# Optimization experiments

Hardware: AMD Instinct MI355X
Metric: run time of the kernel (lower is better)

## Reference

```python
import jax, jax.numpy as jnp
import numpy as np

IN_CH, OUT_CH = 32, 32
MX, MY = 16, 16


def setup_inputs() -> dict:
    key = jax.random.key(0)
    kx, k1r, k1i, k2r, k2i = jax.random.split(key, 5)
    scale = 1.0 / (IN_CH * OUT_CH)
    x = jax.random.normal(kx, (16, IN_CH, 256, 256), dtype=jnp.float32)
    w_shape = (IN_CH, OUT_CH, MX, MY)
    # complex weights stored as real/imag float32 pairs (torch.randn(cfloat) draws
    # independent normal real and imaginary parts)
    w1_real = jax.random.normal(k1r, w_shape, dtype=jnp.float32) * scale
    w1_imag = jax.random.normal(k1i, w_shape, dtype=jnp.float32) * scale
    w2_real = jax.random.normal(k2r, w_shape, dtype=jnp.float32) * scale
    w2_imag = jax.random.normal(k2i, w_shape, dtype=jnp.float32) * scale
    return {"x": x, "w1_real": w1_real, "w1_imag": w1_imag,
            "w2_real": w2_real, "w2_imag": w2_imag}


def reference(x, w1_real, w1_imag, w2_real, w2_imag):
    b, c_in, gx, gy = x.shape
    w1 = w1_real + 1j * w1_imag  # [Cin, Cout, MX, MY]
    w2 = w2_real + 1j * w2_imag
    x_ft = jnp.fft.rfft2(x, axes=(-2, -1))  # [B, Cin, gx, gy//2+1] complex
    # fused complex channel mixing over retained modes (replaces Cin*Cout loop)
    top = jnp.einsum('bixy,ioxy->boxy', x_ft[:, :, :MX, :MY], w1)
    bot = jnp.einsum('bixy,ioxy->boxy', x_ft[:, :, -MX:, :MY], w2)
    out_ft = jnp.zeros((b, OUT_CH, gx, gy // 2 + 1), dtype=x_ft.dtype)
    out_ft = out_ft.at[:, :, :MX, :MY].set(top)
    out_ft = out_ft.at[:, :, -MX:, :MY].set(bot)
    return jnp.fft.irfft2(out_ft, s=(gx, gy), axes=(-2, -1)).astype(x.dtype)
```

## Files before the change

### kernel.cpp

```cpp
#include <hip/hip_runtime.h>
#include <math.h>

#define B     16
#define CIN   32
#define COUT  32
#define G     256
#define NSITE 512

__device__ __forceinline__ int swz8(int bid, int nwg) {
    int q = nwg >> 3;
    return (bid & 7) * q + (bid >> 3);
}

__global__ __launch_bounds__(256, 2) void k_fwd(const float* __restrict__ x,
                                                float2* __restrict__ X) {
    __shared__ float2 tw[256];
    __shared__ float tile[32][257];
    __shared__ float2 T[256][17];
    const int t = threadIdx.x;
    {
        double ang = (double)t * (M_PI / 128.0);
        tw[t] = make_float2((float)cos(ang), (float)sin(ang));
    }
    const int img = blockIdx.x;
    const float* xp = x + (size_t)img * (G * G);

    float ar[16], ai[16], wr[16], wi[16], sr[16], si[16];
    #pragma unroll
    for (int k = 0; k < 16; ++k) { ar[k] = 0.f; ai[k] = 0.f; }
    __syncthreads();
    #pragma unroll
    for (int k = 0; k < 16; ++k) { sr[k] = tw[k].x; si[k] = -tw[k].y; }

    const int row0 = t >> 3, seg = t & 7;
    float4 rs[8];
    #pragma unroll
    for (int p = 0; p < 8; ++p)
        rs[p] = *reinterpret_cast<const float4*>(xp + (size_t)(p * 32 + row0) * G + seg * 4);
    #pragma unroll
    for (int p = 0; p < 8; ++p) {
        int cc = seg * 4, rr = p * 32 + row0;
        tile[cc + 0][rr] = rs[p].x; tile[cc + 1][rr] = rs[p].y;
        tile[cc + 2][rr] = rs[p].z; tile[cc + 3][rr] = rs[p].w;
    }
    __syncthreads();

    for (int c = 0; c < 8; ++c) {
        const int ny0 = c * 32;
        if (c < 7) {
            #pragma unroll
            for (int p = 0; p < 8; ++p)
                rs[p] = *reinterpret_cast<const float4*>(
                    xp + (size_t)(p * 32 + row0) * G + (ny0 + 32) + seg * 4);
        }
        #pragma unroll
        for (int k = 0; k < 16; ++k) {
            float2 w0 = tw[(k * ny0) & 255];
            wr[k] = w0.x; wi[k] = -w0.y;
        }
        for (int j = 0; j < 32; ++j) {
            float xv = tile[j][t];
            #pragma unroll
            for (int k = 0; k < 16; ++k) {
                ar[k] = fmaf(xv, wr[k], ar[k]);
                ai[k] = fmaf(xv, wi[k], ai[k]);
                float nr = fmaf(wr[k], sr[k], -wi[k] * si[k]);
                wi[k]    = fmaf(wr[k], si[k],  wi[k] * sr[k]);
                wr[k] = nr;
            }
        }
        __syncthreads();
        if (c < 7) {
            #pragma unroll
            for (int p = 0; p < 8; ++p) {
                int cc = seg * 4, rr = p * 32 + row0;
                tile[cc + 0][rr] = rs[p].x; tile[cc + 1][rr] = rs[p].y;
                tile[cc + 2][rr] = rs[p].z; tile[cc + 3][rr] = rs[p].w;
            }
            __syncthreads();
        }
    }
    #pragma unroll
    for (int k = 0; k < 16; ++k) T[t][k] = make_float2(ar[k], ai[k]);
    __syncthreads();

    const int ky = t & 15, kxg = t >> 4;
    float x1r = 0.f, x1i = 0.f, x2r = 0.f, x2i = 0.f;
    float w1r = 1.f, w1i = 0.f, w2r = 1.f, w2i = 0.f;
    const float s1r = tw[kxg].x,      s1i = -tw[kxg].y;
    const float s2r = tw[16 - kxg].x, s2i =  tw[16 - kxg].y;
    for (int c = 0; c < 8; ++c) {
        const int nx0 = c * 32;
        {
            int e1 = (kxg * nx0) & 255;
            w1r = tw[e1].x; w1i = -tw[e1].y;
            int e2 = ((16 - kxg) * nx0) & 255;
            w2r = tw[e2].x; w2i = tw[e2].y;
        }
        for (int j = 0; j < 32; ++j) {
            float2 tv = T[nx0 + j][ky];
            x1r = fmaf(tv.x, w1r, fmaf(-tv.y, w1i, x1r));
            x1i = fmaf(tv.x, w1i, fmaf( tv.y, w1r, x1i));
            x2r = fmaf(tv.x, w2r, fmaf(-tv.y, w2i, x2r));
            x2i = fmaf(tv.x, w2i, fmaf( tv.y, w2r, x2i));
            float n1 = fmaf(w1r, s1r, -w1i * s1i);
            w1i      = fmaf(w1r, s1i,  w1i * s1r);
            w1r = n1;
            float n2 = fmaf(w2r, s2r, -w2i * s2i);
            w2i      = fmaf(w2r, s2i,  w2i * s2r);
            w2r = n2;
        }
    }
    float2* Xp = X + (size_t)img * NSITE;
    Xp[kxg * 16 + ky]        = make_float2(x1r, x1i);
    Xp[(kxg + 16) * 16 + ky] = make_float2(x2r, x2i);
}

__global__ __launch_bounds__(256) void k_mix(const float2* __restrict__ X,
                                             const float* __restrict__ w1r,
                                             const float* __restrict__ w1i,
                                             const float* __restrict__ w2r,
                                             const float* __restrict__ w2i,
                                             float2* __restrict__ Y) {
    __shared__ float2 Ws[CIN][COUT];
    __shared__ float2 Xs[B][CIN];
    const int t = threadIdx.x;
    const int site = swz8(blockIdx.x, NSITE);
    const int kxi = site >> 4, kky = site & 15;
    const float* wr; const float* wi; int kxl;
    if (kxi < 16) { wr = w1r; wi = w1i; kxl = kxi; }
    else          { wr = w2r; wi = w2i; kxl = kxi - 16; }
    const int wofs = kxl * 16 + kky;
    for (int p = t; p < CIN * COUT; p += 256)
        Ws[p >> 5][p & 31] = make_float2(wr[p * 256 + wofs], wi[p * 256 + wofs]);
    for (int p = t; p < B * CIN; p += 256) {
        int bb = p >> 5, i = p & 31;
        Xs[bb][i] = X[(size_t)(bb * CIN + i) * NSITE + site];
    }
    __syncthreads();
    for (int p = t; p < B * COUT; p += 256) {
        int bb = p >> 5, o = p & 31;
        float yr = 0.f, yi = 0.f;
        #pragma unroll
        for (int i = 0; i < CIN; ++i) {
            float2 xv = Xs[bb][i];
            float2 wv = Ws[i][o];
            yr = fmaf(xv.x, wv.x, fmaf(-xv.y, wv.y, yr));
            yi = fmaf(xv.x, wv.y, fmaf( xv.y, wv.x, yi));
        }
        Y[(size_t)(bb * COUT + o) * NSITE + site] = make_float2(yr, yi);
    }
}

__global__ __launch_bounds__(256, 2) void k_inv(const float2* __restrict__ Y,
                                                float* __restrict__ out) {
    __shared__ float2 tw[256];
    __shared__ float2 Ys[32][16];
    __shared__ float2 U[256][18];
    const int t = threadIdx.x;
    {
        double ang = (double)t * (M_PI / 128.0);
        tw[t] = make_float2((float)cos(ang), (float)sin(ang));
    }
    const int img = blockIdx.x;
    const float2* yp = Y + (size_t)img * NSITE;
    reinterpret_cast<float4*>(Ys)[t] = reinterpret_cast<const float4*>(yp)[t];
    __syncthreads();

    float ur[16], ui[16];
    #pragma unroll
    for (int k = 0; k < 16; ++k) { ur[k] = 0.f; ui[k] = 0.f; }
    const float str = tw[t].x, sti = tw[t].y;
    float wr = 1.f, wi = 0.f;
    #pragma unroll 2
    for (int kxi = 0; kxi < 16; ++kxi) {
        const float4* yrow = reinterpret_cast<const float4*>(Ys[kxi]);
        #pragma unroll
        for (int q = 0; q < 8; ++q) {
            float4 v = yrow[q];
            ur[2*q]   = fmaf(v.x, wr, fmaf(-v.y, wi, ur[2*q]));
            ui[2*q]   = fmaf(v.x, wi, fmaf( v.y, wr, ui[2*q]));
            ur[2*q+1] = fmaf(v.z, wr, fmaf(-v.w, wi, ur[2*q+1]));
            ui[2*q+1] = fmaf(v.z, wi, fmaf( v.w, wr, ui[2*q+1]));
        }
        float nr = fmaf(wr, str, -wi * sti);
        wi       = fmaf(wr, sti,  wi * str);
        wr = nr;
    }
    {
        int e = (16 * t) & 255;
        wr = tw[e].x; wi = -tw[e].y;
    }
    #pragma unroll 2
    for (int kxi = 16; kxi < 32; ++kxi) {
        const float4* yrow = reinterpret_cast<const float4*>(Ys[kxi]);
        #pragma unroll
        for (int q = 0; q < 8; ++q) {
            float4 v = yrow[q];
            ur[2*q]   = fmaf(v.x, wr, fmaf(-v.y, wi, ur[2*q]));
            ui[2*q]   = fmaf(v.x, wi, fmaf( v.y, wr, ui[2*q]));
            ur[2*q+1] = fmaf(v.z, wr, fmaf(-v.w, wi, ur[2*q+1]));
            ui[2*q+1] = fmaf(v.z, wi, fmaf( v.w, wr, ui[2*q+1]));
        }
        float nr = fmaf(wr, str, -wi * sti);
        wi       = fmaf(wr, sti,  wi * str);
        wr = nr;
    }
    #pragma unroll
    for (int k = 0; k < 16; ++k) U[t][k] = make_float2(ur[k], ui[k]);
    __syncthreads();

    const int wv = t >> 6, ln = t & 63;
    float tc[16], ts[16];
    #pragma unroll
    for (int k = 1; k < 16; ++k) {
        float2 w = tw[(k * ln) & 255];
        tc[k] = 2.f * w.x; ts[k] = 2.f * w.y;
    }
    float* op = out + (size_t)img * (G * G);
    for (int r = 0; r < 64; ++r) {
        const int nx = wv * 64 + r;
        float4 u[8];
        #pragma unroll
        for (int q = 0; q < 8; ++q)
            u[q] = reinterpret_cast<const float4*>(U[nx])[q];
        #pragma unroll
        for (int nb = 0; nb < 4; ++nb) {
            float acc = u[0].x;
            #pragma unroll
            for (int k = 1; k < 16; ++k) {
                float urk = (k & 1) ? u[k >> 1].z : u[k >> 1].x;
                float uik = (k & 1) ? u[k >> 1].w : u[k >> 1].y;
                const int m = (k * nb) & 3;
                if (m == 0)      acc = fmaf(urk, tc[k], fmaf(-uik, ts[k], acc));
                else if (m == 1) acc = fmaf(-urk, ts[k], fmaf(-uik, tc[k], acc));
                else if (m == 2) acc = fmaf(-urk, tc[k], fmaf( uik, ts[k], acc));
                else             acc = fmaf( urk, ts[k], fmaf( uik, tc[k], acc));
            }
            op[(size_t)nx * G + nb * 64 + ln] = acc * (1.0f / 65536.0f);
        }
    }
}

extern "C" void kernel_launch(void* const* d_in, const int* in_sizes, int n_in,
                              void* d_out, int out_size, void* d_ws, size_t ws_size,
                              hipStream_t stream) {
    const float* x   = (const float*)d_in[0];
    const float* w1r = (const float*)d_in[1];
    const float* w1i = (const float*)d_in[2];
    const float* w2r = (const float*)d_in[3];
    const float* w2i = (const float*)d_in[4];
    float* out = (float*)d_out;

    float2* X = (float2*)d_ws;
    float2* Y = X + (size_t)B * CIN * NSITE;

    k_fwd<<<dim3(B * CIN),  dim3(256), 0, stream>>>(x, X);
    k_mix<<<dim3(NSITE),    dim3(256), 0, stream>>>(X, w1r, w1i, w2r, w2i, Y);
    k_inv<<<dim3(B * COUT), dim3(256), 0, stream>>>(Y, out);
}
```

Before: 324.6 us.

## Fold DFT symmetries in forward pass and split inverse kernel across four blocks

The forward row DFT now pairs columns n and n+128 into even/odd sums, so each thread does half the twiddle multiply-accumulates per column. The column DFT pairs rows nx and nx+128 with a sign, which halves the loop. The inverse kernel is split into four blocks per image, each handling 64 output rows, with less register state and a higher occupancy hint. This is meant to cut VALU work and raise parallelism. The cost is more index arithmetic, and the small Y load plus twiddle setup is now repeated four times per image.

```diff
diff --git a/kernel.cpp b/kernel.cpp
--- a/kernel.cpp
+++ b/kernel.cpp
@@ -25,47 +25,55 @@
     const int img = blockIdx.x;
     const float* xp = x + (size_t)img * (G * G);
 
-    float ar[16], ai[16], wr[16], wi[16], sr[16], si[16];
-    #pragma unroll
-    for (int k = 0; k < 16; ++k) { ar[k] = 0.f; ai[k] = 0.f; }
-    __syncthreads();
-    #pragma unroll
-    for (int k = 0; k < 16; ++k) { sr[k] = tw[k].x; si[k] = -tw[k].y; }
-
-    const int row0 = t >> 3, seg = t & 7;
+    float tr[16], ti[16], wr[16], wi[16], sr[16], si[16];
+    #pragma unroll
+    for (int k = 0; k < 16; ++k) { tr[k] = 0.f; ti[k] = 0.f; }
+    __syncthreads();
+    #pragma unroll
+    for (int k = 1; k < 16; ++k) { sr[k] = tw[k].x; si[k] = -tw[k].y; }
+
     float4 rs[8];
     #pragma unroll
-    for (int p = 0; p < 8; ++p)
-        rs[p] = *reinterpret_cast<const float4*>(xp + (size_t)(p * 32 + row0) * G + seg * 4);
-    #pragma unroll
     for (int p = 0; p < 8; ++p) {
-        int cc = seg * 4, rr = p * 32 + row0;
-        tile[cc + 0][rr] = rs[p].x; tile[cc + 1][rr] = rs[p].y;
-        tile[cc + 2][rr] = rs[p].z; tile[cc + 3][rr] = rs[p].w;
+        int idx = p * 256 + t, nx = idx >> 3, sub = idx & 7, h = sub >> 2, q = sub & 3;
+        rs[p] = *reinterpret_cast<const float4*>(xp + (size_t)nx * G + (128 * h + 4 * q));
+    }
+    #pragma unroll
+    for (int p = 0; p < 8; ++p) {
+        int idx = p * 256 + t, nx = idx >> 3, sub = idx & 7, h = sub >> 2, q = sub & 3;
+        int r = 16 * h + 4 * q;
+        tile[r + 0][nx] = rs[p].x; tile[r + 1][nx] = rs[p].y;
+        tile[r + 2][nx] = rs[p].z; tile[r + 3][nx] = rs[p].w;
     }
     __syncthreads();
 
     for (int c = 0; c < 8; ++c) {
-        const int ny0 = c * 32;
+        const int m0 = c * 16;
         if (c < 7) {
             #pragma unroll
-            for (int p = 0; p < 8; ++p)
+            for (int p = 0; p < 8; ++p) {
+                int idx = p * 256 + t, nx = idx >> 3, sub = idx & 7, h = sub >> 2, q = sub & 3;
                 rs[p] = *reinterpret_cast<const float4*>(
-                    xp + (size_t)(p * 32 + row0) * G + (ny0 + 32) + seg * 4);
-        }
-        #pragma unroll
-        for (int k = 0; k < 16; ++k) {
-            float2 w0 = tw[(k * ny0) & 255];
+                    xp + (size_t)nx * G + (m0 + 16 + 128 * h + 4 * q));
+            }
+        }
+        #pragma unroll
+        for (int k = 1; k < 16; ++k) {
+            float2 w0 = tw[(k * m0) & 255];
             wr[k] = w0.x; wi[k] = -w0.y;
         }
-        for (int j = 0; j < 32; ++j) {
-            float xv = tile[j][t];
-            #pragma unroll
-            for (int k = 0; k < 16; ++k) {
-                ar[k] = fmaf(xv, wr[k], ar[k]);
-                ai[k] = fmaf(xv, wi[k], ai[k]);
+        #pragma unroll
+        for (int e = 0; e < 16; ++e) {
+            float x0 = tile[e][t], x1 = tile[16 + e][t];
+            float ev = x0 + x1, od = x0 - x1;
+            tr[0] += ev;
+            #pragma unroll
+            for (int k = 1; k < 16; ++k) {
+                float s_ = (k & 1) ? od : ev;
+                tr[k] = fmaf(s_, wr[k], tr[k]);
+                ti[k] = fmaf(s_, wi[k], ti[k]);
                 float nr = fmaf(wr[k], sr[k], -wi[k] * si[k]);
-                wi[k]    = fmaf(wr[k], si[k],  wi[k] * sr[k]);
+                wi[k]   = fmaf(wr[k], si[k],  wi[k] * sr[k]);
                 wr[k] = nr;
             }
         }
@@ -73,42 +81,45 @@
         if (c < 7) {
             #pragma unroll
             for (int p = 0; p < 8; ++p) {
-                int cc = seg * 4, rr = p * 32 + row0;
-                tile[cc + 0][rr] = rs[p].x; tile[cc + 1][rr] = rs[p].y;
-                tile[cc + 2][rr] = rs[p].z; tile[cc + 3][rr] = rs[p].w;
+                int idx = p * 256 + t, nx = idx >> 3, sub = idx & 7, h = sub >> 2, q = sub & 3;
+                int r = 16 * h + 4 * q;
+                tile[r + 0][nx] = rs[p].x; tile[r + 1][nx] = rs[p].y;
+                tile[r + 2][nx] = rs[p].z; tile[r + 3][nx] = rs[p].w;
             }
             __syncthreads();
         }
     }
     #pragma unroll
-    for (int k = 0; k < 16; ++k) T[t][k] = make_float2(ar[k], ai[k]);
+    for (int k = 0; k < 16; ++k) T[t][k] = make_float2(tr[k], ti[k]);
     __syncthreads();
 
     const int ky = t & 15, kxg = t >> 4;
     float x1r = 0.f, x1i = 0.f, x2r = 0.f, x2i = 0.f;
-    float w1r = 1.f, w1i = 0.f, w2r = 1.f, w2i = 0.f;
+    const float sgn = 1.f - 2.f * (float)(kxg & 1);
     const float s1r = tw[kxg].x,      s1i = -tw[kxg].y;
     const float s2r = tw[16 - kxg].x, s2i =  tw[16 - kxg].y;
-    for (int c = 0; c < 8; ++c) {
-        const int nx0 = c * 32;
-        {
-            int e1 = (kxg * nx0) & 255;
-            w1r = tw[e1].x; w1i = -tw[e1].y;
-            int e2 = ((16 - kxg) * nx0) & 255;
-            w2r = tw[e2].x; w2i = tw[e2].y;
-        }
+    for (int c2 = 0; c2 < 4; ++c2) {
+        const int nx0 = c2 * 32;
+        int e1 = (kxg * nx0) & 255;
+        float w1r_ = tw[e1].x, w1i_ = -tw[e1].y;
+        int e2 = ((16 - kxg) * nx0) & 255;
+        float w2r_ = tw[e2].x, w2i_ = tw[e2].y;
+        #pragma unroll
         for (int j = 0; j < 32; ++j) {
-            float2 tv = T[nx0 + j][ky];
-            x1r = fmaf(tv.x, w1r, fmaf(-tv.y, w1i, x1r));
-            x1i = fmaf(tv.x, w1i, fmaf( tv.y, w1r, x1i));
-            x2r = fmaf(tv.x, w2r, fmaf(-tv.y, w2i, x2r));
-            x2i = fmaf(tv.x, w2i, fmaf( tv.y, w2r, x2i));
-            float n1 = fmaf(w1r, s1r, -w1i * s1i);
-            w1i      = fmaf(w1r, s1i,  w1i * s1r);
-            w1r = n1;
-            float n2 = fmaf(w2r, s2r, -w2i * s2i);
-            w2i      = fmaf(w2r, s2i,  w2i * s2r);
-            w2r = n2;
+            float2 a = T[nx0 + j][ky];
+            float2 b = T[128 + nx0 + j][ky];
+            float pr = fmaf(sgn, b.x, a.x);
+            float pi = fmaf(sgn, b.y, a.y);
+            x1r = fmaf(pr, w1r_, fmaf(-pi, w1i_, x1r));
+            x1i = fmaf(pr, w1i_, fmaf( pi, w1r_, x1i));
+            x2r = fmaf(pr, w2r_, fmaf(-pi, w2i_, x2r));
+            x2i = fmaf(pr, w2i_, fmaf( pi, w2r_, x2i));
+            float n1 = fmaf(w1r_, s1r, -w1i_ * s1i);
+            w1i_     = fmaf(w1r_, s1i,  w1i_ * s1r);
+            w1r_ = n1;
+            float n2 = fmaf(w2r_, s2r, -w2i_ * s2i);
+            w2i_     = fmaf(w2r_, s2i,  w2i_ * s2r);
+            w2r_ = n2;
         }
     }
     float2* Xp = X + (size_t)img * NSITE;
@@ -152,62 +163,54 @@
     }
 }
 
-__global__ __launch_bounds__(256, 2) void k_inv(const float2* __restrict__ Y,
+__global__ __launch_bounds__(256, 4) void k_inv(const float2* __restrict__ Y,
                                                 float* __restrict__ out) {
     __shared__ float2 tw[256];
-    __shared__ float2 Ys[32][16];
-    __shared__ float2 U[256][18];
+    __shared__ __align__(16) float2 Ys[32][16];
+    __shared__ __align__(16) float2 U[64][18];
     const int t = threadIdx.x;
     {
         double ang = (double)t * (M_PI / 128.0);
         tw[t] = make_float2((float)cos(ang), (float)sin(ang));
     }
-    const int img = blockIdx.x;
+    const int img = blockIdx.x >> 2, Q = blockIdx.x & 3;
     const float2* yp = Y + (size_t)img * NSITE;
     reinterpret_cast<float4*>(Ys)[t] = reinterpret_cast<const float4*>(yp)[t];
     __syncthreads();
 
-    float ur[16], ui[16];
-    #pragma unroll
-    for (int k = 0; k < 16; ++k) { ur[k] = 0.f; ui[k] = 0.f; }
-    const float str = tw[t].x, sti = tw[t].y;
+    const int nxl = t & 63, kg = t >> 6;
+    const int nx = Q * 64 + nxl;
+    float ur[4], ui[4];
+    #pragma unroll
+    for (int j = 0; j < 4; ++j) { ur[j] = 0.f; ui[j] = 0.f; }
+    const float str = tw[nx].x, sti = tw[nx].y;
     float wr = 1.f, wi = 0.f;
-    #pragma unroll 2
+    #pragma unroll 4
     for (int kxi = 0; kxi < 16; ++kxi) {
-        const float4* yrow = reinterpret_cast<const float4*>(Ys[kxi]);
-        #pragma unroll
-        for (int q = 0; q < 8; ++q) {
-            float4 v = yrow[q];
-            ur[2*q]   = fmaf(v.x, wr, fmaf(-v.y, wi, ur[2*q]));
-            ui[2*q]   = fmaf(v.x, wi, fmaf( v.y, wr, ui[2*q]));
-            ur[2*q+1] = fmaf(v.z, wr, fmaf(-v.w, wi, ur[2*q+1]));
-            ui[2*q+1] = fmaf(v.z, wi, fmaf( v.w, wr, ui[2*q+1]));
-        }
-        float nr = fmaf(wr, str, -wi * sti);
-        wi       = fmaf(wr, sti,  wi * str);
-        wr = nr;
+        float4 a = reinterpret_cast<const float4*>(Ys[kxi])[2 * kg];
+        float4 b = reinterpret_cast<const float4*>(Ys[kxi])[2 * kg + 1];
+        ur[0] = fmaf(a.x, wr, fmaf(-a.y, wi, ur[0])); ui[0] = fmaf(a.x, wi, fmaf(a.y, wr, ui[0]));
+        ur[1] = fmaf(a.z, wr, fmaf(-a.w, wi, ur[1])); ui[1] = fmaf(a.z, wi, fmaf(a.w, wr, ui[1]));
+        ur[2] = fmaf(b.x, wr, fmaf(-b.y, wi, ur[2])); ui[2] = fmaf(b.x, wi, fmaf(b.y, wr, ui[2]));
+        ur[3] = fmaf(b.z, wr, fmaf(-b.w, wi, ur[3])); ui[3] = fmaf(b.z, wi, fmaf(b.w, wr, ui[3]));
+        float nr = fmaf(wr, str, -wi * sti); wi = fmaf(wr, sti, wi * str); wr = nr;
     }
     {
-        int e = (16 * t) & 255;
+        int e = (16 * nx) & 255;
         wr = tw[e].x; wi = -tw[e].y;
     }
-    #pragma unroll 2
+    #pragma unroll 4
     for (int kxi = 16; kxi < 32; ++kxi) {
-        const float4* yrow = reinterpret_cast<const float4*>(Ys[kxi]);
-        #pragma unroll
-        for (int q = 0; q < 8; ++q) {
-            float4 v = yrow[q];
-            ur[2*q]   = fmaf(v.x, wr, fmaf(-v.y, wi, ur[2*q]));
-            ui[2*q]   = fmaf(v.x, wi, fmaf( v.y, wr, ui[2*q]));
-            ur[2*q+1] = fmaf(v.z, wr, fmaf(-v.w, wi, ur[2*q+1]));
-            ui[2*q+1] = fmaf(v.z, wi, fmaf( v.w, wr, ui[2*q+1]));
-        }
-        float nr = fmaf(wr, str, -wi * sti);
-        wi       = fmaf(wr, sti,  wi * str);
-        wr = nr;
-    }
-    #pragma unroll
-    for (int k = 0; k < 16; ++k) U[t][k] = make_float2(ur[k], ui[k]);
+        float4 a = reinterpret_cast<const float4*>(Ys[kxi])[2 * kg];
+        float4 b = reinterpret_cast<const float4*>(Ys[kxi])[2 * kg + 1];
+        ur[0] = fmaf(a.x, wr, fmaf(-a.y, wi, ur[0])); ui[0] = fmaf(a.x, wi, fmaf(a.y, wr, ui[0]));
+        ur[1] = fmaf(a.z, wr, fmaf(-a.w, wi, ur[1])); ui[1] = fmaf(a.z, wi, fmaf(a.w, wr, ui[1]));
+        ur[2] = fmaf(b.x, wr, fmaf(-b.y, wi, ur[2])); ui[2] = fmaf(b.x, wi, fmaf(b.y, wr, ui[2]));
+        ur[3] = fmaf(b.z, wr, fmaf(-b.w, wi, ur[3])); ui[3] = fmaf(b.z, wi, fmaf(b.w, wr, ui[3]));
+        float nr = fmaf(wr, str, -wi * sti); wi = fmaf(wr, sti, wi * str); wr = nr;
+    }
+    #pragma unroll
+    for (int j = 0; j < 4; ++j) U[nxl][4 * kg + j] = make_float2(ur[j], ui[j]);
     __syncthreads();
 
     const int wv = t >> 6, ln = t & 63;
@@ -218,12 +221,13 @@
         tc[k] = 2.f * w.x; ts[k] = 2.f * w.y;
     }
     float* op = out + (size_t)img * (G * G);
-    for (int r = 0; r < 64; ++r) {
-        const int nx = wv * 64 + r;
+    for (int r = 0; r < 16; ++r) {
+        const int rl = wv * 16 + r;
+        const int nxg = Q * 64 + rl;
         float4 u[8];
         #pragma unroll
         for (int q = 0; q < 8; ++q)
-            u[q] = reinterpret_cast<const float4*>(U[nx])[q];
+            u[q] = reinterpret_cast<const float4*>(U[rl])[q];
         #pragma unroll
         for (int nb = 0; nb < 4; ++nb) {
             float acc = u[0].x;
@@ -237,7 +241,7 @@
                 else if (m == 2) acc = fmaf(-urk, tc[k], fmaf( uik, ts[k], acc));
                 else             acc = fmaf( urk, ts[k], fmaf( uik, tc[k], acc));
             }
-            op[(size_t)nx * G + nb * 64 + ln] = acc * (1.0f / 65536.0f);
+            op[(size_t)nxg * G + nb * 64 + ln] = acc * (1.0f / 65536.0f);
         }
     }
 }
@@ -255,7 +259,7 @@
     float2* X = (float2*)d_ws;
     float2* Y = X + (size_t)B * CIN * NSITE;
 
-    k_fwd<<<dim3(B * CIN),  dim3(256), 0, stream>>>(x, X);
-    k_mix<<<dim3(NSITE),    dim3(256), 0, stream>>>(X, w1r, w1i, w2r, w2i, Y);
-    k_inv<<<dim3(B * COUT), dim3(256), 0, stream>>>(Y, out);
-}
+    k_fwd<<<dim3(B * CIN),      dim3(256), 0, stream>>>(x, X);
+    k_mix<<<dim3(NSITE),        dim3(256), 0, stream>>>(X, w1r, w1i, w2r, w2i, Y);
+    k_inv<<<dim3(B * COUT * 4), dim3(256), 0, stream>>>(Y, out);
+}
```

After: 304.9 us. 6.1% less time.
